# Performance work log

Measured on AMD Instinct MI355X. Metric: run time of the kernel, lower is better.

The kernel has to match this reference:

```python
import jax, jax.numpy as jnp
import numpy as np
import math

N, T, D, H = 64, 256, 768, 256

def setup_inputs() -> dict:
    key = jax.random.key(0)
    ks = jax.random.split(key, 5)
    s = 0.02
    return {
        "x": jax.random.normal(ks[0], (N, T, D), dtype=jnp.float32),
        "Wq": jax.random.normal(ks[1], (H, D), dtype=jnp.float32) * s,
        "Wk": jax.random.normal(ks[2], (H, D), dtype=jnp.float32) * s,
        "Wv": jax.random.normal(ks[3], (H, D), dtype=jnp.float32) * s,
        "Wo": jax.random.normal(ks[4], (D, H), dtype=jnp.float32) * s,
    }

def reference(x, Wq, Wk, Wv, Wo):
    # flatten [N,T,D] -> [M,D], full self-attention over all M tokens
    n, t, d = x.shape
    xf = x.reshape(n * t, d)                      # [M, D]
    q = xf @ Wq.T                                  # [M, H]
    k = xf @ Wk.T                                  # [M, H]
    v = xf @ Wv.T                                  # [M, H]
    scale = 1.0 / math.sqrt(q.shape[-1])
    att = jax.nn.softmax((q @ k.T) * scale, axis=-1)  # [M, M]
    pooled = (att @ v) @ Wo.T                      # [M, D]
    return pooled.mean(axis=0, keepdims=True)      # [1, D]
```

## Files before the change

### kernel.cpp

```cpp
#include <hip/hip_runtime.h>


typedef unsigned short u16;
typedef __attribute__((ext_vector_type(8))) unsigned short u16x8;
typedef __bf16 bf16x8 __attribute__((ext_vector_type(8)));
typedef float f32x4 __attribute__((ext_vector_type(4)));

#define MTOK 16384
#define DDIM 768
#define HDIM 256
#define SM_SCALE 0.0625f

#define OFF_XB    (size_t)0
#define OFF_WCAT  (size_t)25165824
#define OFF_QB    (size_t)26345472
#define OFF_KB    (size_t)34734080
#define OFF_VF    (size_t)43122688
#define OFF_RS    (size_t)59899904
#define OFF_RINV  (size_t)59965440
#define OFF_CA    (size_t)60030976
#define OFF_P     (size_t)60096512
#define WS_NEED   (size_t)60097536

__device__ __forceinline__ u16 f2bf(float f) {
  union { float f; unsigned u; } v; v.f = f;
  unsigned r = v.u + 0x7fffu + ((v.u >> 16) & 1u);
  return (u16)(r >> 16);
}

__global__ void k_conv(const float* __restrict__ src, u16* __restrict__ dst, int n8) {
  int i = blockIdx.x * blockDim.x + threadIdx.x;
  if (i >= n8) return;
  const float4* s = (const float4*)src;
  float4 a = s[2 * i], b = s[2 * i + 1];
  u16x8 o = { f2bf(a.x), f2bf(a.y), f2bf(a.z), f2bf(a.w),
              f2bf(b.x), f2bf(b.y), f2bf(b.z), f2bf(b.w) };
  *(u16x8*)(dst + (size_t)i * 8) = o;
}

__device__ __forceinline__ void stage_tile(const u16* __restrict__ g, int ld,
                                           u16* lds, int wid, int lane) {
  const int r = lane >> 2;
  const int c = (lane & 3) * 8;
#pragma unroll
  for (int i = 0; i < 2; ++i) {
    int ii = wid * 2 + i;
    const u16* gp = g + (size_t)(ii * 16 + r) * ld + c;
    __builtin_amdgcn_global_load_lds(
        (const __attribute__((address_space(1))) unsigned int*)gp,
        (__attribute__((address_space(3))) unsigned int*)(lds + ii * 512),
        16, 0, 0);
  }
}

#define KSTEP(APTR, LDA, BPTR, LDB)                                           \
  {                                                                           \
    stage_tile((APTR), (LDA), As, wid, lane);                                 \
    stage_tile((BPTR), (LDB), Bs, wid, lane);                                 \
    __syncthreads();                                                          \
    bf16x8 af[4], bfr[4];                                                     \
    const int kk = (lane >> 4) * 8;                                           \
    _Pragma("unroll") for (int m = 0; m < 4; ++m)                             \
        af[m] = *(const bf16x8*)(As + (wm * 64 + m * 16 + (lane & 15)) * 32 + kk); \
    _Pragma("unroll") for (int n = 0; n < 4; ++n)                             \
        bfr[n] = *(const bf16x8*)(Bs + (wn * 64 + n * 16 + (lane & 15)) * 32 + kk); \
    _Pragma("unroll") for (int m = 0; m < 4; ++m)                             \
        _Pragma("unroll") for (int n = 0; n < 4; ++n)                         \
            acc[m][n] = __builtin_amdgcn_mfma_f32_16x16x32_bf16(              \
                af[m], bfr[n], acc[m][n], 0, 0, 0);                           \
    __syncthreads();                                                          \
  }

__global__ __launch_bounds__(256, 2) void k_qkv(const u16* __restrict__ Xb,
                                                const u16* __restrict__ Wcat,
                                                u16* __restrict__ Qb,
                                                u16* __restrict__ Kb,
                                                float* __restrict__ Vf) {
  __shared__ u16 As[128 * 32];
  __shared__ u16 Bs[128 * 32];
  const int tid = threadIdx.x, wid = tid >> 6, lane = tid & 63;
  const int wm = wid >> 1, wn = wid & 1;
  const int row0 = blockIdx.x * 128;
  const int col0 = blockIdx.y * 128;
  f32x4 acc[4][4] = {};
  for (int k0 = 0; k0 < DDIM; k0 += 32) {
    KSTEP(Xb + (size_t)row0 * DDIM + k0, DDIM,
          Wcat + (size_t)col0 * DDIM + k0, DDIM);
  }
#pragma unroll
  for (int m = 0; m < 4; ++m)
#pragma unroll
    for (int n = 0; n < 4; ++n) {
      int col = col0 + wn * 64 + n * 16 + (lane & 15);
#pragma unroll
      for (int j = 0; j < 4; ++j) {
        int row = row0 + wm * 64 + m * 16 + (lane >> 4) * 4 + j;
        float v = acc[m][n][j];
        if (col < 256)      Qb[(size_t)row * HDIM + col]         = f2bf(v);
        else if (col < 512) Kb[(size_t)row * HDIM + (col - 256)] = f2bf(v);
        else                Vf[(size_t)row * HDIM + (col - 512)] = v;
      }
    }
}


__device__ __forceinline__ void stage_kt(u16* sh, const u16* __restrict__ Qb,
                                         const u16* __restrict__ Kb,
                                         int rp, int cg, int wid, int srow,
                                         int wsrc, int t) {
  const int kb = (t & 3) * 128;
  u16* dst = sh + (t & 1) * 32768;
  if (wid < 4) {
    const char* base = (const char*)Qb + (size_t)(rp * 256) * 512 + kb + wsrc;
#pragma unroll
    for (int j = 0; j < 8; ++j) {
      int c = wid * 8 + j;
      int row = c * 8 + srow;
      __builtin_amdgcn_global_load_lds(
          (const __attribute__((address_space(1))) unsigned int*)(base + (size_t)row * 512),
          (__attribute__((address_space(3))) unsigned int*)(dst + c * 512),
          16, 0, 0);
    }
  } else {
    const int ct = cg * 8 + (t >> 2);
    const char* base = (const char*)Kb + (size_t)(ct * 256) * 512 + kb + wsrc;
#pragma unroll
    for (int j = 0; j < 8; ++j) {
      int c = (wid - 4) * 8 + j;
      int row = c * 8 + srow;
      __builtin_amdgcn_global_load_lds(
          (const __attribute__((address_space(1))) unsigned int*)(base + (size_t)row * 512),
          (__attribute__((address_space(3))) unsigned int*)(dst + 16384 + c * 512),
          16, 0, 0);
    }
  }
}

template <int PASS>
__global__ __launch_bounds__(512, 2) void k_spass(const u16* __restrict__ Qb,
                                                  const u16* __restrict__ Kb,
                                                  const float* __restrict__ rinv,
                                                  float* __restrict__ dst) {
  __shared__ u16 sh[65536];
  const int tid = threadIdx.x, wid = tid >> 6, lane = tid & 63;
  const int wm = wid >> 2, wn = wid & 3;
  const int rp = blockIdx.x >> 3;
  const int cg = blockIdx.x & 7;

  const int colp = (lane >> 4) * 16;
  const int swzr = (lane & 7) << 4;
  const int rd0 = ((0  + colp) ^ swzr) >> 1;
  const int rd1 = ((64 + colp) ^ swzr) >> 1;
  const int srow = lane >> 3;
  const int wsrc = ((lane & 7) ^ srow) << 4;

  f32x4 acc[8][4] = {};
  float aux[8][4];
#pragma unroll
  for (int mi = 0; mi < 8; ++mi)
#pragma unroll
    for (int j = 0; j < 4; ++j)
      aux[mi][j] = (PASS == 1) ? 0.0f
          : rinv[rp * 256 + wm * 128 + mi * 16 + (lane >> 4) * 4 + j];

  stage_kt(sh, Qb, Kb, rp, cg, wid, srow, wsrc, 0);

  for (int t = 0; t < 32; ++t) {
    if (t + 1 < 32) {
      stage_kt(sh, Qb, Kb, rp, cg, wid, srow, wsrc, t + 1);
      asm volatile("s_waitcnt vmcnt(8)" ::: "memory");
    } else {
      asm volatile("s_waitcnt vmcnt(0)" ::: "memory");
    }
    __builtin_amdgcn_s_barrier();

    const int base = (t & 1) * 32768;
    const u16* Ab = sh + base;
    const u16* Bb = sh + base + 16384;

    bf16x8 bq[4][2];
#pragma unroll
    for (int ni = 0; ni < 4; ++ni) {
      const int rb = (wn * 64 + ni * 16 + (lane & 15)) * 64;
      bq[ni][0] = *(const bf16x8*)(Bb + rb + rd0);
      bq[ni][1] = *(const bf16x8*)(Bb + rb + rd1);
    }
    __builtin_amdgcn_s_setprio(1);
#pragma unroll
    for (int mi = 0; mi < 8; ++mi) {
      const int ra = (wm * 128 + mi * 16 + (lane & 15)) * 64;
      bf16x8 a0 = *(const bf16x8*)(Ab + ra + rd0);
      bf16x8 a1 = *(const bf16x8*)(Ab + ra + rd1);
#pragma unroll
      for (int ni = 0; ni < 4; ++ni) {
        acc[mi][ni] = __builtin_amdgcn_mfma_f32_16x16x32_bf16(a0, bq[ni][0], acc[mi][ni], 0, 0, 0);
        acc[mi][ni] = __builtin_amdgcn_mfma_f32_16x16x32_bf16(a1, bq[ni][1], acc[mi][ni], 0, 0, 0);
      }
    }
    __builtin_amdgcn_s_setprio(0);
    __builtin_amdgcn_s_barrier();

    if ((t & 3) == 3) {
      if (PASS == 1) {
#pragma unroll
        for (int mi = 0; mi < 8; ++mi)
#pragma unroll
          for (int ni = 0; ni < 4; ++ni)
#pragma unroll
            for (int j = 0; j < 4; ++j)
              aux[mi][j] += __expf(acc[mi][ni][j] * SM_SCALE);
      } else {
        const int ct = cg * 8 + (t >> 2);
        float cs[4] = {};
#pragma unroll
        for (int mi = 0; mi < 8; ++mi)
#pragma unroll
          for (int ni = 0; ni < 4; ++ni)
#pragma unroll
            for (int j = 0; j < 4; ++j)
              cs[ni] += __expf(acc[mi][ni][j] * SM_SCALE) * aux[mi][j];
#pragma unroll
        for (int ni = 0; ni < 4; ++ni) {
          float v = cs[ni];
          v += __shfl_xor(v, 16);
          v += __shfl_xor(v, 32);
          if ((lane >> 4) == 0)
            atomicAdd(&dst[ct * 256 + wn * 64 + ni * 16 + (lane & 15)], v);
        }
      }
#pragma unroll
      for (int mi = 0; mi < 8; ++mi)
#pragma unroll
        for (int ni = 0; ni < 4; ++ni)
          acc[mi][ni] = (f32x4){0.f, 0.f, 0.f, 0.f};
    }
  }

  if (PASS == 1) {
#pragma unroll
    for (int mi = 0; mi < 8; ++mi)
#pragma unroll
      for (int j = 0; j < 4; ++j) {
        float v = aux[mi][j];
        v += __shfl_xor(v, 1);  v += __shfl_xor(v, 2);
        v += __shfl_xor(v, 4);  v += __shfl_xor(v, 8);
        if ((lane & 15) == 0)
          atomicAdd(&dst[rp * 256 + wm * 128 + mi * 16 + (lane >> 4) * 4 + j], v);
      }
  }
}

__global__ void k_rinv(const float* __restrict__ rowsum, float* __restrict__ rinv) {
  int i = blockIdx.x * 256 + threadIdx.x;
  if (i < MTOK) rinv[i] = 1.0f / (rowsum[i] * (float)MTOK);
}

__global__ void k_p(const float* __restrict__ colacc, const float* __restrict__ Vf,
                    float* __restrict__ p) {
  const int h = threadIdx.x;
  const int r0 = blockIdx.x * 128;
  float s = 0.f;
  for (int r = r0; r < r0 + 128; ++r)
    s += colacc[r] * Vf[(size_t)r * HDIM + h];
  atomicAdd(&p[h], s);
}

__global__ void k_out(const float* __restrict__ p, const float* __restrict__ Wo,
                      float* __restrict__ out) {
  const int d = blockIdx.x * 256 + threadIdx.x;
  if (d >= DDIM) return;
  float s = 0.f;
  for (int h = 0; h < HDIM; ++h) s += p[h] * Wo[(size_t)d * HDIM + h];
  out[d] = s;
}

extern "C" void kernel_launch(void* const* d_in, const int* in_sizes, int n_in,
                              void* d_out, int out_size, void* d_ws, size_t ws_size,
                              hipStream_t stream) {
  const float* x  = (const float*)d_in[0];
  const float* Wq = (const float*)d_in[1];
  const float* Wk = (const float*)d_in[2];
  const float* Wv = (const float*)d_in[3];
  const float* Wo = (const float*)d_in[4];
  float* out = (float*)d_out;

  char* ws = (char*)d_ws;
  u16*   Xb     = (u16*)(ws + OFF_XB);
  u16*   Wcat   = (u16*)(ws + OFF_WCAT);
  u16*   Qb     = (u16*)(ws + OFF_QB);
  u16*   Kb     = (u16*)(ws + OFF_KB);
  float* Vf     = (float*)(ws + OFF_VF);
  float* rowsum = (float*)(ws + OFF_RS);
  float* rinv   = (float*)(ws + OFF_RINV);
  float* colacc = (float*)(ws + OFF_CA);
  float* p      = (float*)(ws + OFF_P);

  k_conv<<<(MTOK * DDIM / 8 + 255) / 256, 256, 0, stream>>>(x, Xb, MTOK * DDIM / 8);
  const int w8 = HDIM * DDIM / 8;
  k_conv<<<(w8 + 255) / 256, 256, 0, stream>>>(Wq, Wcat + 0 * HDIM * DDIM, w8);
  k_conv<<<(w8 + 255) / 256, 256, 0, stream>>>(Wk, Wcat + 1 * HDIM * DDIM, w8);
  k_conv<<<(w8 + 255) / 256, 256, 0, stream>>>(Wv, Wcat + 2 * HDIM * DDIM, w8);

  hipMemsetAsync(ws + OFF_RS, 0, WS_NEED - OFF_RS, stream);

  k_qkv<<<dim3(MTOK / 128, DDIM / 128), 256, 0, stream>>>(Xb, Wcat, Qb, Kb, Vf);

  k_spass<1><<<512, 512, 0, stream>>>(Qb, Kb, nullptr, rowsum);
  k_rinv<<<MTOK / 256, 256, 0, stream>>>(rowsum, rinv);
  k_spass<2><<<512, 512, 0, stream>>>(Qb, Kb, rinv, colacc);

  k_p<<<MTOK / 128, 256, 0, stream>>>(colacc, Vf, p);
  k_out<<<(DDIM + 255) / 256, 256, 0, stream>>>(p, Wo, out);
}
```

Baseline: 536.5 us.

## Keep Q row-panel resident in LDS and stream only K tiles

The score-pass kernel now loads the block's full 256x256 bf16 Q panel into LDS once, with an XOR swizzle, instead of re-staging Q chunks alongside K on every step. Only K is double-buffered, in 32-wide k-slices over 64 steps. This removes the repeated Q traffic from global/L2 and halves per-step staging. In exchange it raises LDS use to 160 KB per block, makes the initial Q load unoverlapped, and doubles the number of barriers for the same amount of work.

```diff
diff --git a/kernel.cpp b/kernel.cpp
--- a/kernel.cpp
+++ b/kernel.cpp
@@ -5,6 +5,9 @@
 typedef __attribute__((ext_vector_type(8))) unsigned short u16x8;
 typedef __bf16 bf16x8 __attribute__((ext_vector_type(8)));
 typedef float f32x4 __attribute__((ext_vector_type(4)));
+
+#define AS1 __attribute__((address_space(1)))
+#define AS3 __attribute__((address_space(3)))
 
 #define MTOK 16384
 #define DDIM 768
@@ -46,10 +49,8 @@
   for (int i = 0; i < 2; ++i) {
     int ii = wid * 2 + i;
     const u16* gp = g + (size_t)(ii * 16 + r) * ld + c;
-    __builtin_amdgcn_global_load_lds(
-        (const __attribute__((address_space(1))) unsigned int*)gp,
-        (__attribute__((address_space(3))) unsigned int*)(lds + ii * 512),
-        16, 0, 0);
+    __builtin_amdgcn_global_load_lds((const AS1 unsigned int*)gp,
+                                     (AS3 unsigned int*)(lds + ii * 512), 16, 0, 0);
   }
 }
 
@@ -104,55 +105,25 @@
 }
 
 
-__device__ __forceinline__ void stage_kt(u16* sh, const u16* __restrict__ Qb,
-                                         const u16* __restrict__ Kb,
-                                         int rp, int cg, int wid, int srow,
-                                         int wsrc, int t) {
-  const int kb = (t & 3) * 128;
-  u16* dst = sh + (t & 1) * 32768;
-  if (wid < 4) {
-    const char* base = (const char*)Qb + (size_t)(rp * 256) * 512 + kb + wsrc;
-#pragma unroll
-    for (int j = 0; j < 8; ++j) {
-      int c = wid * 8 + j;
-      int row = c * 8 + srow;
-      __builtin_amdgcn_global_load_lds(
-          (const __attribute__((address_space(1))) unsigned int*)(base + (size_t)row * 512),
-          (__attribute__((address_space(3))) unsigned int*)(dst + c * 512),
-          16, 0, 0);
-    }
-  } else {
-    const int ct = cg * 8 + (t >> 2);
-    const char* base = (const char*)Kb + (size_t)(ct * 256) * 512 + kb + wsrc;
-#pragma unroll
-    for (int j = 0; j < 8; ++j) {
-      int c = (wid - 4) * 8 + j;
-      int row = c * 8 + srow;
-      __builtin_amdgcn_global_load_lds(
-          (const __attribute__((address_space(1))) unsigned int*)(base + (size_t)row * 512),
-          (__attribute__((address_space(3))) unsigned int*)(dst + 16384 + c * 512),
-          16, 0, 0);
-    }
-  }
-}
-
 template <int PASS>
 __global__ __launch_bounds__(512, 2) void k_spass(const u16* __restrict__ Qb,
                                                   const u16* __restrict__ Kb,
                                                   const float* __restrict__ rinv,
                                                   float* __restrict__ dst) {
-  __shared__ u16 sh[65536];
+  __shared__ u16 sh[81920];
   const int tid = threadIdx.x, wid = tid >> 6, lane = tid & 63;
   const int wm = wid >> 2, wn = wid & 3;
   const int rp = blockIdx.x >> 3;
   const int cg = blockIdx.x & 7;
 
-  const int colp = (lane >> 4) * 16;
-  const int swzr = (lane & 7) << 4;
-  const int rd0 = ((0  + colp) ^ swzr) >> 1;
-  const int rd1 = ((64 + colp) ^ swzr) >> 1;
-  const int srow = lane >> 3;
-  const int wsrc = ((lane & 7) ^ srow) << 4;
+  const int l15 = lane & 15;
+  const int akey = (lane & 7) << 4;
+  const int bkey = ((l15 ^ (l15 >> 2)) & 3) << 4;
+  const int bcol = (((lane >> 4) * 16) ^ bkey) >> 1;
+  const int a_srow = lane >> 5;
+  const int a_scol = (lane & 31) * 16;
+  const int b_srow = lane >> 2;
+  const int b_scol = ((lane & 3) * 16) ^ ((((lane >> 2) & 3) ^ ((lane >> 4) & 3)) << 4);
 
   f32x4 acc[8][4] = {};
   float aux[8][4];
@@ -163,44 +134,63 @@
       aux[mi][j] = (PASS == 1) ? 0.0f
           : rinv[rp * 256 + wm * 128 + mi * 16 + (lane >> 4) * 4 + j];
 
-  stage_kt(sh, Qb, Kb, rp, cg, wid, srow, wsrc, 0);
-
-  for (int t = 0; t < 32; ++t) {
-    if (t + 1 < 32) {
-      stage_kt(sh, Qb, Kb, rp, cg, wid, srow, wsrc, t + 1);
-      asm volatile("s_waitcnt vmcnt(8)" ::: "memory");
+  {
+    const char* gA = (const char*)Qb + (size_t)(rp * 256) * 512;
+#pragma unroll
+    for (int j = 0; j < 16; ++j) {
+      const int i = wid * 16 + j;
+      const int row = i * 2 + a_srow;
+      const char* src = gA + (size_t)row * 512 + (a_scol ^ ((row & 7) << 4));
+      __builtin_amdgcn_global_load_lds((const AS1 unsigned int*)src,
+                                       (AS3 unsigned int*)(sh + i * 512), 16, 0, 0);
+    }
+  }
+
+#define STAGE_B(S)                                                            \
+  {                                                                           \
+    const int ct_ = cg * 8 + ((S) >> 3), t_ = (S) & 7;                        \
+    const char* gB = (const char*)Kb + (size_t)(ct_ * 256) * 512 + t_ * 64;   \
+    u16* dl = sh + 65536 + ((S) & 1) * 8192;                                  \
+    _Pragma("unroll") for (int j = 0; j < 2; ++j) {                           \
+      const int i = wid * 2 + j;                                              \
+      const char* src = gB + (size_t)(i * 16 + b_srow) * 512 + b_scol;        \
+      __builtin_amdgcn_global_load_lds((const AS1 unsigned int*)src,          \
+                                       (AS3 unsigned int*)(dl + i * 512), 16, 0, 0); \
+    }                                                                         \
+  }
+
+  STAGE_B(0);
+
+  for (int s = 0; s < 64; ++s) {
+    if (s + 1 < 64) {
+      STAGE_B(s + 1);
+      asm volatile("s_waitcnt vmcnt(2)" ::: "memory");
     } else {
       asm volatile("s_waitcnt vmcnt(0)" ::: "memory");
     }
     __builtin_amdgcn_s_barrier();
 
-    const int base = (t & 1) * 32768;
-    const u16* Ab = sh + base;
-    const u16* Bb = sh + base + 16384;
-
-    bf16x8 bq[4][2];
-#pragma unroll
-    for (int ni = 0; ni < 4; ++ni) {
-      const int rb = (wn * 64 + ni * 16 + (lane & 15)) * 64;
-      bq[ni][0] = *(const bf16x8*)(Bb + rb + rd0);
-      bq[ni][1] = *(const bf16x8*)(Bb + rb + rd1);
-    }
+    const int t = s & 7;
+    const u16* Bb = sh + 65536 + (s & 1) * 8192;
+    const int acolt = ((t * 64 + (lane >> 4) * 16) ^ akey) >> 1;
+
+    bf16x8 bq[4];
+#pragma unroll
+    for (int ni = 0; ni < 4; ++ni)
+      bq[ni] = *(const bf16x8*)(Bb + (wn * 64 + ni * 16 + l15) * 32 + bcol);
+
     __builtin_amdgcn_s_setprio(1);
 #pragma unroll
     for (int mi = 0; mi < 8; ++mi) {
-      const int ra = (wm * 128 + mi * 16 + (lane & 15)) * 64;
-      bf16x8 a0 = *(const bf16x8*)(Ab + ra + rd0);
-      bf16x8 a1 = *(const bf16x8*)(Ab + ra + rd1);
-#pragma unroll
-      for (int ni = 0; ni < 4; ++ni) {
-        acc[mi][ni] = __builtin_amdgcn_mfma_f32_16x16x32_bf16(a0, bq[ni][0], acc[mi][ni], 0, 0, 0);
-        acc[mi][ni] = __builtin_amdgcn_mfma_f32_16x16x32_bf16(a1, bq[ni][1], acc[mi][ni], 0, 0, 0);
-      }
+      bf16x8 a0 = *(const bf16x8*)(sh + (wm * 128 + mi * 16 + l15) * 256 + acolt);
+#pragma unroll
+      for (int ni = 0; ni < 4; ++ni)
+        acc[mi][ni] = __builtin_amdgcn_mfma_f32_16x16x32_bf16(a0, bq[ni], acc[mi][ni], 0, 0, 0);
     }
     __builtin_amdgcn_s_setprio(0);
     __builtin_amdgcn_s_barrier();
 
-    if ((t & 3) == 3) {
+    if ((s & 7) == 7) {
       if (PASS == 1) {
 #pragma unroll
         for (int mi = 0; mi < 8; ++mi)
@@ -210,7 +200,7 @@
             for (int j = 0; j < 4; ++j)
               aux[mi][j] += __expf(acc[mi][ni][j] * SM_SCALE);
       } else {
-        const int ct = cg * 8 + (t >> 2);
+        const int ct = cg * 8 + (s >> 3);
         float cs[4] = {};
 #pragma unroll
         for (int mi = 0; mi < 8; ++mi)
@@ -225,7 +215,7 @@
           v += __shfl_xor(v, 16);
           v += __shfl_xor(v, 32);
           if ((lane >> 4) == 0)
-            atomicAdd(&dst[ct * 256 + wn * 64 + ni * 16 + (lane & 15)], v);
+            atomicAdd(&dst[ct * 256 + wn * 64 + ni * 16 + l15], v);
         }
       }
 #pragma unroll
@@ -244,7 +234,7 @@
         float v = aux[mi][j];
         v += __shfl_xor(v, 1);  v += __shfl_xor(v, 2);
         v += __shfl_xor(v, 4);  v += __shfl_xor(v, 8);
-        if ((lane & 15) == 0)
+        if (l15 == 0)
           atomicAdd(&dst[rp * 256 + wm * 128 + mi * 16 + (lane >> 4) * 4 + j], v);
       }
   }
```

Measured after the change: 455.7 us. -15.1%, faster.
